# Kernel optimization log

Hardware: AMD Instinct MI355X
Metric: run time of the kernel (lower is better)

Reference implementation:

```python
import jax, jax.numpy as jnp
import numpy as np

N_HEADS = 4
DIM_HEAD = 32
SCALE = DIM_HEAD ** -0.5
EPS = 1e-5


def setup_inputs() -> dict:
    key = jax.random.key(0)
    ks = jax.random.split(key, 5)
    b, dim, l, h, w = 8, 128, 32, 32, 32
    hidden = N_HEADS * DIM_HEAD  # 128
    return {
        "x": jax.random.normal(ks[0], (b, dim, l, h, w), dtype=jnp.float32),
        "w_qkv": jax.random.normal(ks[1], (3 * hidden, dim), dtype=jnp.float32) * 0.05,
        "w_out": jax.random.normal(ks[2], (dim, hidden), dtype=jnp.float32) * 0.05,
        "b_out": jax.random.normal(ks[3], (dim,), dtype=jnp.float32) * 0.05,
        "gn_gamma": jnp.ones((dim,), dtype=jnp.float32),
        "gn_beta": jnp.zeros((dim,), dtype=jnp.float32),
    }


def reference(x, w_qkv, w_out, b_out, gn_gamma, gn_beta):
    b, dim, l, h_sp, w_sp = x.shape
    n = l * h_sp * w_sp
    hidden = N_HEADS * DIM_HEAD
    xf = x.reshape(b, dim, n)  # flatten spatial -> tokens
    # 1x1 conv == channel matmul: [3*hidden, dim] x [b, dim, n]
    qkv = jnp.einsum('oc,bcn->bon', w_qkv, xf)
    qkv = qkv.reshape(b, 3, N_HEADS, DIM_HEAD, n)
    q, k, v = qkv[:, 0], qkv[:, 1], qkv[:, 2]  # each [b, H, d, n]
    q = jax.nn.softmax(q, axis=2) * SCALE      # softmax over feature dim d
    k = jax.nn.softmax(k, axis=-1)             # softmax over tokens n
    c = jnp.einsum('bhdn,bhen->bhde', k, v)    # [b, H, d, e] tiny context
    out = jnp.einsum('bhde,bhdn->bhen', c, q)  # [b, H, e, n]
    out = out.reshape(b, hidden, n)
    # to_out 1x1 conv + bias
    y = jnp.einsum('oc,bcn->bon', w_out, out) + b_out[None, :, None]
    # GroupNorm(1, dim): normalize over (C, spatial) per sample
    mean = jnp.mean(y, axis=(1, 2), keepdims=True)
    var = jnp.var(y, axis=(1, 2), keepdims=True)
    y = (y - mean) * jax.lax.rsqrt(var + EPS)
    y = y * gn_gamma[None, :, None] + gn_beta[None, :, None]
    return y.reshape(b, dim, l, h_sp, w_sp)
```

## Files before the change

### kernel.cpp

```cpp
#include <hip/hip_runtime.h>

#define BATCH 8
#define DIMC 128
#define NTOT 32768
#define HEADS 4
#define DHEAD 32
#define SCALE_Q 0.17677669529663687f

typedef _Float16 half8  __attribute__((ext_vector_type(8)));
typedef _Float16 half4v __attribute__((ext_vector_type(4)));
typedef _Float16 half2v __attribute__((ext_vector_type(2)));
typedef float    f32x4  __attribute__((ext_vector_type(4)));

#define WS_WQKV 0
#define WS_WOUT 98304
#define WS_S    131072
#define WS_Z    262144
#define WS_ST   266240
#define WS_CT   266304
#define WS_NEED 331840

__global__ void k0_prep(const float* __restrict__ wqkv, const float* __restrict__ wout,
                        char* __restrict__ ws) {
    int i = blockIdx.x * 256 + threadIdx.x;
    _Float16* Wb = (_Float16*)(ws + WS_WQKV);
    _Float16* Wo = (_Float16*)(ws + WS_WOUT);
    float* S  = (float*)(ws + WS_S);
    float* Z  = (float*)(ws + WS_Z);
    float* St = (float*)(ws + WS_ST);
    if (i < 49152) Wb[i] = (_Float16)wqkv[i];
    int j = i - 49152;
    if (j >= 0 && j < 16384) Wo[j] = (_Float16)wout[j];
    int k = j - 16384;
    if (k >= 0 && k < 32768) S[k] = 0.f;
    int m = k - 32768;
    if (m >= 0 && m < 1024) Z[m] = 0.f;
    int s = m - 1024;
    if (s >= 0 && s < 16) St[s] = 0.f;
}

__global__ __launch_bounds__(256, 2) void k1_kv(const float* __restrict__ x,
                                                const _Float16* __restrict__ Wb,
                                                float* __restrict__ S,
                                                float* __restrict__ Z) {
    __shared__ _Float16 Xb[64][136];
    __shared__ _Float16 KB[128][64];
    __shared__ _Float16 VB[128][64];
    const int t = threadIdx.x;
    const int lane = t & 63, w = t >> 6, g = lane >> 4, l15 = lane & 15;
    const int b = blockIdx.y;

    half8 af[4][4];
#pragma unroll
    for (int mt = 0; mt < 4; ++mt)
#pragma unroll
        for (int kc = 0; kc < 4; ++kc)
            af[mt][kc] = *(const half8*)(Wb + (size_t)(128 + (w * 4 + mt) * 16 + l15) * 128 + kc * 32 + 8 * g);

    f32x4 sacc[2][2];
#pragma unroll
    for (int dm = 0; dm < 2; ++dm)
#pragma unroll
        for (int en = 0; en < 2; ++en) sacc[dm][en] = (f32x4){0.f, 0.f, 0.f, 0.f};
    float zpart = 0.f;

    const int j4 = t & 15, c0 = t >> 4;
    const int sxw = (j4 & 7) << 3;

    float4 xr[8];
#pragma unroll
    for (int cc = 0; cc < 8; ++cc)
        xr[cc] = *(const float4*)(x + ((size_t)b * DIMC + c0 + 16 * cc) * NTOT + blockIdx.x * 64 + 4 * j4);
#pragma unroll
    for (int cc = 0; cc < 8; ++cc) {
        const int c = c0 + 16 * cc;
        Xb[4 * j4 + 0][c ^ sxw] = (_Float16)xr[cc].x;
        Xb[4 * j4 + 1][c ^ sxw] = (_Float16)xr[cc].y;
        Xb[4 * j4 + 2][c ^ sxw] = (_Float16)xr[cc].z;
        Xb[4 * j4 + 3][c ^ sxw] = (_Float16)xr[cc].w;
    }

    for (int it = 0; it < 8; ++it) {
        if (it < 7) {
            const int j0n = (blockIdx.x + 64 * (it + 1)) * 64;
#pragma unroll
            for (int cc = 0; cc < 8; ++cc)
                xr[cc] = *(const float4*)(x + ((size_t)b * DIMC + c0 + 16 * cc) * NTOT + j0n + 4 * j4);
        }
        __syncthreads();
        half8 bf[4][4];
#pragma unroll
        for (int nt = 0; nt < 4; ++nt) {
            const int sb = ((4 * nt + (l15 >> 2)) & 7) << 3;
#pragma unroll
            for (int kc = 0; kc < 4; ++kc)
                bf[nt][kc] = *(const half8*)(&Xb[nt * 16 + l15][(kc * 32 + 8 * g) ^ sb]);
        }
#pragma unroll
        for (int mt = 0; mt < 4; ++mt) {
            f32x4 a0 = (f32x4){0.f,0.f,0.f,0.f}, a1 = a0, a2 = a0, a3 = a0;
#pragma unroll
            for (int kc = 0; kc < 4; ++kc) {
                a0 = __builtin_amdgcn_mfma_f32_16x16x32_f16(af[mt][kc], bf[0][kc], a0, 0, 0, 0);
                a1 = __builtin_amdgcn_mfma_f32_16x16x32_f16(af[mt][kc], bf[1][kc], a1, 0, 0, 0);
                a2 = __builtin_amdgcn_mfma_f32_16x16x32_f16(af[mt][kc], bf[2][kc], a2, 0, 0, 0);
                a3 = __builtin_amdgcn_mfma_f32_16x16x32_f16(af[mt][kc], bf[3][kc], a3, 0, 0, 0);
            }
            const int lr0 = (w * 4 + mt) * 16 + g * 4;
            const int skv = (((w * 4 + mt) * 4 + g) & 7) << 3;
#pragma unroll
            for (int nt = 0; nt < 4; ++nt) {
                const f32x4 a = (nt == 0) ? a0 : (nt == 1) ? a1 : (nt == 2) ? a2 : a3;
                const int jn = (nt * 16 + l15) ^ skv;
                if (lr0 < 128) {
#pragma unroll
                    for (int r = 0; r < 4; ++r) KB[lr0 + r][jn] = (_Float16)__expf(a[r]);
                } else {
#pragma unroll
                    for (int r = 0; r < 4; ++r) VB[lr0 - 128 + r][jn] = (_Float16)a[r];
                }
            }
        }
        __syncthreads();
        if (it < 7) {
#pragma unroll
            for (int cc = 0; cc < 8; ++cc) {
                const int c = c0 + 16 * cc;
                Xb[4 * j4 + 0][c ^ sxw] = (_Float16)xr[cc].x;
                Xb[4 * j4 + 1][c ^ sxw] = (_Float16)xr[cc].y;
                Xb[4 * j4 + 2][c ^ sxw] = (_Float16)xr[cc].z;
                Xb[4 * j4 + 3][c ^ sxw] = (_Float16)xr[cc].w;
            }
        }
#pragma unroll
        for (int dm = 0; dm < 2; ++dm) {
            const int sr = ((4 * dm + (l15 >> 2)) & 7) << 3;
#pragma unroll
            for (int en = 0; en < 2; ++en)
#pragma unroll
                for (int kc = 0; kc < 2; ++kc) {
                    half8 ka = *(const half8*)(&KB[w * 32 + dm * 16 + l15][(kc * 32 + 8 * g) ^ sr]);
                    half8 vb = *(const half8*)(&VB[w * 32 + en * 16 + l15][(kc * 32 + 8 * g) ^ sr]);
                    sacc[dm][en] = __builtin_amdgcn_mfma_f32_16x16x32_f16(ka, vb, sacc[dm][en], 0, 0, 0);
                }
        }
        {
            const int zr = lane >> 1;
            const int sz = ((zr >> 2) & 7) << 3;
#pragma unroll
            for (int s8 = 0; s8 < 4; ++s8) {
                half8 hv = *(const half8*)(&KB[w * 32 + zr][((lane & 1) * 32 + 8 * s8) ^ sz]);
#pragma unroll
                for (int e = 0; e < 8; ++e) zpart += (float)hv[e];
            }
        }
    }
    {
        float zt = zpart + __shfl_xor(zpart, 1);
        if ((lane & 1) == 0) atomicAdd(&Z[(b * HEADS + w) * DHEAD + (lane >> 1)], zt);
    }
#pragma unroll
    for (int dm = 0; dm < 2; ++dm)
#pragma unroll
        for (int en = 0; en < 2; ++en)
#pragma unroll
            for (int r = 0; r < 4; ++r)
                atomicAdd(&S[((size_t)(b * HEADS + w) * DHEAD + dm * 16 + g * 4 + r) * DHEAD + en * 16 + l15],
                          sacc[dm][en][r]);
}

__global__ void k2_ct(const float* __restrict__ S, const float* __restrict__ Z,
                      _Float16* __restrict__ CT) {
    int i = blockIdx.x * 256 + threadIdx.x;
    int d = i & 31, e = (i >> 5) & 31, bh = i >> 10;
    CT[i] = (_Float16)(S[(bh * 32 + d) * 32 + e] / Z[bh * 32 + d]);
}

__global__ __launch_bounds__(256, 2) void k3_main(const float* __restrict__ x,
                                                  const _Float16* __restrict__ Wb,
                                                  const _Float16* __restrict__ Wo,
                                                  const _Float16* __restrict__ CT,
                                                  const float* __restrict__ b_out,
                                                  char* __restrict__ ybase,
                                                  float* __restrict__ St) {
    __shared__ _Float16 Xb[64][136];
    __shared__ _Float16 qT[64][136];
    __shared__ _Float16 oT[64][136];
    __shared__ float scl[4][64];
    __shared__ float red[8];
    const int t = threadIdx.x;
    const int lane = t & 63, w = t >> 6, g = lane >> 4, l15 = lane & 15;
    const int b = blockIdx.y;
    const int j4 = t & 15, c0 = t >> 4;
    const int sxw = (j4 & 7) << 3;

    half8 wa[2][4];
#pragma unroll
    for (int mi = 0; mi < 2; ++mi)
#pragma unroll
        for (int kc = 0; kc < 4; ++kc)
            wa[mi][kc] = *(const half8*)(Wb + (size_t)((w * 2 + mi) * 16 + l15) * 128 + kc * 32 + 8 * g);
    half8 ca[2];
#pragma unroll
    for (int et = 0; et < 2; ++et)
        ca[et] = *(const half8*)(CT + ((size_t)(b * HEADS + w) * DHEAD + et * 16 + l15) * DHEAD + 8 * g);

    float ssum = 0.f, ssq = 0.f;

    float4 xr[8];
#pragma unroll
    for (int cc = 0; cc < 8; ++cc)
        xr[cc] = *(const float4*)(x + ((size_t)b * DIMC + c0 + 16 * cc) * NTOT + blockIdx.x * 64 + 4 * j4);
#pragma unroll
    for (int cc = 0; cc < 8; ++cc) {
        const int c = c0 + 16 * cc;
        Xb[4 * j4 + 0][c ^ sxw] = (_Float16)xr[cc].x;
        Xb[4 * j4 + 1][c ^ sxw] = (_Float16)xr[cc].y;
        Xb[4 * j4 + 2][c ^ sxw] = (_Float16)xr[cc].z;
        Xb[4 * j4 + 3][c ^ sxw] = (_Float16)xr[cc].w;
    }
    __syncthreads();

    for (int it = 0; it < 8; ++it) {
        const int j0 = (blockIdx.x + 64 * it) * 64;
        if (it < 7) {
            const int j0n = (blockIdx.x + 64 * (it + 1)) * 64;
#pragma unroll
            for (int cc = 0; cc < 8; ++cc)
                xr[cc] = *(const float4*)(x + ((size_t)b * DIMC + c0 + 16 * cc) * NTOT + j0n + 4 * j4);
        }
        {
            half8 bf[4][4];
#pragma unroll
            for (int nt = 0; nt < 4; ++nt) {
                const int sb = ((4 * nt + (l15 >> 2)) & 7) << 3;
#pragma unroll
                for (int kc = 0; kc < 4; ++kc)
                    bf[nt][kc] = *(const half8*)(&Xb[nt * 16 + l15][(kc * 32 + 8 * g) ^ sb]);
            }
            float ps[4] = {0.f, 0.f, 0.f, 0.f};
#pragma unroll
            for (int mi = 0; mi < 2; ++mi) {
                const int mt = w * 2 + mi;
                f32x4 acc[4];
#pragma unroll
                for (int nt = 0; nt < 4; ++nt) acc[nt] = (f32x4){0.f, 0.f, 0.f, 0.f};
#pragma unroll
                for (int kc = 0; kc < 4; ++kc)
#pragma unroll
                    for (int nt = 0; nt < 4; ++nt)
                        acc[nt] = __builtin_amdgcn_mfma_f32_16x16x32_f16(wa[mi][kc], bf[nt][kc], acc[nt], 0, 0, 0);
#pragma unroll
                for (int nt = 0; nt < 4; ++nt) {
                    const int sb = ((4 * nt + (l15 >> 2)) & 7) << 3;
                    half4v p;
#pragma unroll
                    for (int r = 0; r < 4; ++r) {
                        const float e = __expf(acc[nt][r]);
                        ps[nt] += e;
                        p[r] = (_Float16)e;
                    }
                    *(half4v*)(&qT[nt * 16 + l15][(mt * 16 + g * 4) ^ sb]) = p;
                }
            }
#pragma unroll
            for (int nt = 0; nt < 4; ++nt) {
                ps[nt] += __shfl_xor(ps[nt], 16);
                ps[nt] += __shfl_xor(ps[nt], 32);
            }
            if (lane < 16) {
#pragma unroll
                for (int nt = 0; nt < 4; ++nt) scl[w][nt * 16 + lane] = SCALE_Q / ps[nt];
            }
        }
        __syncthreads();
        if (it < 7) {
#pragma unroll
            for (int cc = 0; cc < 8; ++cc) {
                const int c = c0 + 16 * cc;
                Xb[4 * j4 + 0][c ^ sxw] = (_Float16)xr[cc].x;
                Xb[4 * j4 + 1][c ^ sxw] = (_Float16)xr[cc].y;
                Xb[4 * j4 + 2][c ^ sxw] = (_Float16)xr[cc].z;
                Xb[4 * j4 + 3][c ^ sxw] = (_Float16)xr[cc].w;
            }
        }
        {
            half8 bf3[4];
            float sc[4];
#pragma unroll
            for (int nt = 0; nt < 4; ++nt) {
                const int sb = ((4 * nt + (l15 >> 2)) & 7) << 3;
                bf3[nt] = *(const half8*)(&qT[nt * 16 + l15][(w * 32 + 8 * g) ^ sb]);
                sc[nt] = scl[w][nt * 16 + l15];
            }
#pragma unroll
            for (int et = 0; et < 2; ++et) {
                f32x4 acc[4];
#pragma unroll
                for (int nt = 0; nt < 4; ++nt) acc[nt] = (f32x4){0.f, 0.f, 0.f, 0.f};
#pragma unroll
                for (int nt = 0; nt < 4; ++nt)
                    acc[nt] = __builtin_amdgcn_mfma_f32_16x16x32_f16(ca[et], bf3[nt], acc[nt], 0, 0, 0);
#pragma unroll
                for (int nt = 0; nt < 4; ++nt) {
                    const int sb = ((4 * nt + (l15 >> 2)) & 7) << 3;
                    half4v p;
#pragma unroll
                    for (int r = 0; r < 4; ++r) p[r] = (_Float16)(acc[nt][r] * sc[nt]);
                    *(half4v*)(&oT[nt * 16 + l15][(w * 32 + et * 16 + g * 4) ^ sb]) = p;
                }
            }
        }
        __syncthreads();
        {
            half8 bf[4][4];
#pragma unroll
            for (int nt = 0; nt < 4; ++nt) {
                const int sb = ((4 * nt + (l15 >> 2)) & 7) << 3;
#pragma unroll
                for (int kc = 0; kc < 4; ++kc)
                    bf[nt][kc] = *(const half8*)(&oT[nt * 16 + l15][(kc * 32 + 8 * g) ^ sb]);
            }
#pragma unroll
            for (int mi = 0; mi < 2; ++mi) {
                const int mt = w * 2 + mi;
                const int o0 = mt * 16 + g * 4;
                half8 af[4];
#pragma unroll
                for (int kc = 0; kc < 4; ++kc)
                    af[kc] = *(const half8*)(Wo + (size_t)(mt * 16 + l15) * 128 + kc * 32 + 8 * g);
                f32x4 acc[4];
#pragma unroll
                for (int nt = 0; nt < 4; ++nt) acc[nt] = (f32x4){0.f, 0.f, 0.f, 0.f};
#pragma unroll
                for (int kc = 0; kc < 4; ++kc)
#pragma unroll
                    for (int nt = 0; nt < 4; ++nt)
                        acc[nt] = __builtin_amdgcn_mfma_f32_16x16x32_f16(af[kc], bf[nt][kc], acc[nt], 0, 0, 0);
                float bo[4];
#pragma unroll
                for (int r = 0; r < 4; ++r) bo[r] = b_out[o0 + r];
#pragma unroll
                for (int r = 0; r < 4; ++r) {
                    _Float16* yrow = (_Float16*)(ybase + (size_t)(b * DIMC + o0 + r) * 131072 + 65536);
#pragma unroll
                    for (int nt = 0; nt < 4; ++nt) {
                        const int jn = j0 + nt * 16 + l15;
                        const float yv = acc[nt][r] + bo[r];
                        ssum += yv;
                        ssq += yv * yv;
                        yrow[jn] = (_Float16)yv;
                    }
                }
            }
        }
        __syncthreads();
    }
#pragma unroll
    for (int m = 32; m; m >>= 1) { ssum += __shfl_xor(ssum, m); ssq += __shfl_xor(ssq, m); }
    if (lane == 0) { red[w] = ssum; red[4 + w] = ssq; }
    __syncthreads();
    if (t == 0) {
        atomicAdd(&St[b * 2 + 0], red[0] + red[1] + red[2] + red[3]);
        atomicAdd(&St[b * 2 + 1], red[4] + red[5] + red[6] + red[7]);
    }
}

__global__ __launch_bounds__(256) void k4_norm(float* __restrict__ out, const float* __restrict__ St,
                                               const float* __restrict__ gamma,
                                               const float* __restrict__ beta) {
    const int o = blockIdx.x;
    const int b = blockIdx.y;
    const int t = threadIdx.x;
    const size_t row = (size_t)b * DIMC + o;
    const float n = (float)DIMC * (float)NTOT;
    const float mean = St[b * 2] / n;
    const float var = St[b * 2 + 1] / n - mean * mean;
    const float rs = rsqrtf(var + 1e-5f);
    const float ga = gamma[o] * rs;
    const float be = beta[o];
    const half8* yh = (const half8*)((const char*)out + row * 131072 + 65536);
    half8 hbuf[16];
#pragma unroll
    for (int i = 0; i < 16; ++i) hbuf[i] = yh[i * 256 + t];
    __syncthreads();
    float4* orow = (float4*)(out + row * NTOT);
#pragma unroll
    for (int i = 0; i < 16; ++i) {
        const int e4 = (i * 256 + t) * 2;
        float4 v0, v1;
        v0.x = ((float)hbuf[i][0] - mean) * ga + be;
        v0.y = ((float)hbuf[i][1] - mean) * ga + be;
        v0.z = ((float)hbuf[i][2] - mean) * ga + be;
        v0.w = ((float)hbuf[i][3] - mean) * ga + be;
        v1.x = ((float)hbuf[i][4] - mean) * ga + be;
        v1.y = ((float)hbuf[i][5] - mean) * ga + be;
        v1.z = ((float)hbuf[i][6] - mean) * ga + be;
        v1.w = ((float)hbuf[i][7] - mean) * ga + be;
        orow[e4] = v0;
        orow[e4 + 1] = v1;
    }
}

extern "C" void kernel_launch(void* const* d_in, const int* in_sizes, int n_in,
                              void* d_out, int out_size, void* d_ws, size_t ws_size,
                              hipStream_t stream) {
    const float* x     = (const float*)d_in[0];
    const float* wqkv  = (const float*)d_in[1];
    const float* wout  = (const float*)d_in[2];
    const float* b_out = (const float*)d_in[3];
    const float* gamma = (const float*)d_in[4];
    const float* beta  = (const float*)d_in[5];
    if (ws_size < WS_NEED) return;
    char* ws = (char*)d_ws;
    _Float16* Wb = (_Float16*)(ws + WS_WQKV);
    _Float16* Wo = (_Float16*)(ws + WS_WOUT);
    float* S  = (float*)(ws + WS_S);
    float* Z  = (float*)(ws + WS_Z);
    float* St = (float*)(ws + WS_ST);
    _Float16* CT = (_Float16*)(ws + WS_CT);

    k0_prep<<<389, 256, 0, stream>>>(wqkv, wout, ws);
    k1_kv<<<dim3(64, 8), 256, 0, stream>>>(x, Wb, S, Z);
    k2_ct<<<128, 256, 0, stream>>>(S, Z, CT);
    k3_main<<<dim3(64, 8), 256, 0, stream>>>(x, Wb, Wo, CT, b_out, (char*)d_out, St);
    k4_norm<<<dim3(128, 8), 256, 0, stream>>>((float*)d_out, St, gamma, beta);
}
```

Before: 139.3 us.

## Merge qT/oT shared buffers in k3 and double its grid width

Result: slower. 143.9 us (+3.3%).

```diff
diff --git a/kernel.cpp b/kernel.cpp
--- a/kernel.cpp
+++ b/kernel.cpp
@@ -6,6 +6,10 @@
 #define HEADS 4
 #define DHEAD 32
 #define SCALE_Q 0.17677669529663687f
+#define K1_GRIDX 64
+#define K1_TILES 8
+#define K3_GRIDX 128
+#define K3_TILES 4
 
 typedef _Float16 half8  __attribute__((ext_vector_type(8)));
 typedef _Float16 half4v __attribute__((ext_vector_type(4)));
@@ -80,9 +84,9 @@
         Xb[4 * j4 + 3][c ^ sxw] = (_Float16)xr[cc].w;
     }
 
-    for (int it = 0; it < 8; ++it) {
-        if (it < 7) {
-            const int j0n = (blockIdx.x + 64 * (it + 1)) * 64;
+    for (int it = 0; it < K1_TILES; ++it) {
+        if (it < K1_TILES - 1) {
+            const int j0n = (blockIdx.x + K1_GRIDX * (it + 1)) * 64;
 #pragma unroll
             for (int cc = 0; cc < 8; ++cc)
                 xr[cc] = *(const float4*)(x + ((size_t)b * DIMC + c0 + 16 * cc) * NTOT + j0n + 4 * j4);
@@ -122,7 +126,7 @@
             }
         }
         __syncthreads();
-        if (it < 7) {
+        if (it < K1_TILES - 1) {
 #pragma unroll
             for (int cc = 0; cc < 8; ++cc) {
                 const int c = c0 + 16 * cc;
@@ -184,8 +188,7 @@
                                                   char* __restrict__ ybase,
                                                   float* __restrict__ St) {
     __shared__ _Float16 Xb[64][136];
-    __shared__ _Float16 qT[64][136];
-    __shared__ _Float16 oT[64][136];
+    __shared__ _Float16 qoT[64][136];
     __shared__ float scl[4][64];
     __shared__ float red[8];
     const int t = threadIdx.x;
@@ -221,10 +224,10 @@
     }
     __syncthreads();
 
-    for (int it = 0; it < 8; ++it) {
-        const int j0 = (blockIdx.x + 64 * it) * 64;
-        if (it < 7) {
-            const int j0n = (blockIdx.x + 64 * (it + 1)) * 64;
+    for (int it = 0; it < K3_TILES; ++it) {
+        const int j0 = (blockIdx.x + K3_GRIDX * it) * 64;
+        if (it < K3_TILES - 1) {
+            const int j0n = (blockIdx.x + K3_GRIDX * (it + 1)) * 64;
 #pragma unroll
             for (int cc = 0; cc < 8; ++cc)
                 xr[cc] = *(const float4*)(x + ((size_t)b * DIMC + c0 + 16 * cc) * NTOT + j0n + 4 * j4);
@@ -260,7 +263,7 @@
                         ps[nt] += e;
                         p[r] = (_Float16)e;
                     }
-                    *(half4v*)(&qT[nt * 16 + l15][(mt * 16 + g * 4) ^ sb]) = p;
+                    *(half4v*)(&qoT[nt * 16 + l15][(mt * 16 + g * 4) ^ sb]) = p;
                 }
             }
 #pragma unroll
@@ -274,7 +277,7 @@
             }
         }
         __syncthreads();
-        if (it < 7) {
+        if (it < K3_TILES - 1) {
 #pragma unroll
             for (int cc = 0; cc < 8; ++cc) {
                 const int c = c0 + 16 * cc;
@@ -284,31 +287,30 @@
                 Xb[4 * j4 + 3][c ^ sxw] = (_Float16)xr[cc].w;
             }
         }
-        {
-            half8 bf3[4];
-            float sc[4];
+        half8 bf3[4];
+        float sc[4];
+#pragma unroll
+        for (int nt = 0; nt < 4; ++nt) {
+            const int sb = ((4 * nt + (l15 >> 2)) & 7) << 3;
+            bf3[nt] = *(const half8*)(&qoT[nt * 16 + l15][(w * 32 + 8 * g) ^ sb]);
+            sc[nt] = scl[w][nt * 16 + l15];
+        }
+        __syncthreads();
+#pragma unroll
+        for (int et = 0; et < 2; ++et) {
+            f32x4 acc[4];
+#pragma unroll
+            for (int nt = 0; nt < 4; ++nt) acc[nt] = (f32x4){0.f, 0.f, 0.f, 0.f};
+#pragma unroll
+            for (int nt = 0; nt < 4; ++nt)
+                acc[nt] = __builtin_amdgcn_mfma_f32_16x16x32_f16(ca[et], bf3[nt], acc[nt], 0, 0, 0);
 #pragma unroll
             for (int nt = 0; nt < 4; ++nt) {
                 const int sb = ((4 * nt + (l15 >> 2)) & 7) << 3;
-                bf3[nt] = *(const half8*)(&qT[nt * 16 + l15][(w * 32 + 8 * g) ^ sb]);
-                sc[nt] = scl[w][nt * 16 + l15];
-            }
-#pragma unroll
-            for (int et = 0; et < 2; ++et) {
-                f32x4 acc[4];
-#pragma unroll
-                for (int nt = 0; nt < 4; ++nt) acc[nt] = (f32x4){0.f, 0.f, 0.f, 0.f};
-#pragma unroll
-                for (int nt = 0; nt < 4; ++nt)
-                    acc[nt] = __builtin_amdgcn_mfma_f32_16x16x32_f16(ca[et], bf3[nt], acc[nt], 0, 0, 0);
-#pragma unroll
-                for (int nt = 0; nt < 4; ++nt) {
-                    const int sb = ((4 * nt + (l15 >> 2)) & 7) << 3;
-                    half4v p;
-#pragma unroll
-                    for (int r = 0; r < 4; ++r) p[r] = (_Float16)(acc[nt][r] * sc[nt]);
-                    *(half4v*)(&oT[nt * 16 + l15][(w * 32 + et * 16 + g * 4) ^ sb]) = p;
-                }
+                half4v p;
+#pragma unroll
+                for (int r = 0; r < 4; ++r) p[r] = (_Float16)(acc[nt][r] * sc[nt]);
+                *(half4v*)(&qoT[nt * 16 + l15][(w * 32 + et * 16 + g * 4) ^ sb]) = p;
             }
         }
         __syncthreads();
@@ -319,7 +321,7 @@
                 const int sb = ((4 * nt + (l15 >> 2)) & 7) << 3;
 #pragma unroll
                 for (int kc = 0; kc < 4; ++kc)
-                    bf[nt][kc] = *(const half8*)(&oT[nt * 16 + l15][(kc * 32 + 8 * g) ^ sb]);
+                    bf[nt][kc] = *(const half8*)(&qoT[nt * 16 + l15][(kc * 32 + 8 * g) ^ sb]);
             }
 #pragma unroll
             for (int mi = 0; mi < 2; ++mi) {
@@ -421,8 +423,8 @@
     _Float16* CT = (_Float16*)(ws + WS_CT);
 
     k0_prep<<<389, 256, 0, stream>>>(wqkv, wout, ws);
-    k1_kv<<<dim3(64, 8), 256, 0, stream>>>(x, Wb, S, Z);
+    k1_kv<<<dim3(K1_GRIDX, 8), 256, 0, stream>>>(x, Wb, S, Z);
     k2_ct<<<128, 256, 0, stream>>>(S, Z, CT);
-    k3_main<<<dim3(64, 8), 256, 0, stream>>>(x, Wb, Wo, CT, b_out, (char*)d_out, St);
+    k3_main<<<dim3(K3_GRIDX, 8), 256, 0, stream>>>(x, Wb, Wo, CT, b_out, (char*)d_out, St);
     k4_norm<<<dim3(128, 8), 256, 0, stream>>>((float*)d_out, St, gamma, beta);
 }
```
